# Kernel optimization log

Hardware: AMD Instinct MI355X
Metric: run time of the kernel (lower is better)

Reference implementation:

```python
import jax, jax.numpy as jnp
import numpy as np
from jax import lax

B, T, C, F = 64, 1152, 64, 8
L_DP, N_DP = 24, 12
NUM_CLASSES = 4


def setup_inputs() -> dict:
    key = jax.random.key(0)
    ks = jax.random.split(key, 8)
    num_chunks = T // L_DP
    return {
        "L_norm": jax.random.normal(ks[0], (B, C, C), jnp.float32) / C,
        "X_seq": jax.random.normal(ks[1], (B, T, C, F), jnp.float32),
        "deterministic": 1,
        "conv_kernel": jax.random.normal(ks[2], (32, 1, F, 8), jnp.float32) * 0.06,  # HWIO
        "ln_scale": jnp.ones((8,), jnp.float32),
        "ln_bias": jnp.zeros((8,), jnp.float32),
        "spatial_w": jax.random.normal(ks[3], (64, 4), jnp.float32) * 0.17,
        "W1": jax.random.normal(ks[4], (num_chunks * 64, 32), jnp.float32) * 0.02,
        "b1": jnp.zeros((32,), jnp.float32),
        "W2": jax.random.normal(ks[5], (32, NUM_CLASSES), jnp.float32) * 0.1,
        "b2": jnp.zeros((NUM_CLASSES,), jnp.float32),
    }


def _spike(x):
    return jnp.where(x > 0, 1.0, 0.0).astype(x.dtype)


def reference(L_norm, X_seq, deterministic, conv_kernel, ln_scale, ln_bias,
              spatial_w, W1, b1, W2, b2):
    # temporal conv over (T, C) spatial dims, F -> 8 channels, SAME padding
    ann = lax.conv_general_dilated(
        X_seq, conv_kernel, window_strides=(1, 1), padding="SAME",
        dimension_numbers=("NHWC", "HWIO", "NHWC"))
    # LayerNorm over last (feature) axis, eps=1e-6 (flax default)
    mu = jnp.mean(ann, axis=-1, keepdims=True)
    var = jnp.mean(jnp.square(ann - mu), axis=-1, keepdims=True)
    ann = (ann - mu) * lax.rsqrt(var + 1e-6) * ln_scale + ln_bias
    ann = jax.nn.relu(ann)
    # graph propagation + channel-spatial projection
    gx = jnp.einsum("bnm,btmf->btnf", L_norm, ann)          # (B,T,64,8)
    gx_csp = jnp.einsum("btcf,cs->btsf", gx, spatial_w)     # (B,T,4,8)
    snn_in = gx_csp.reshape(B, T, 32)

    # two-layer LIF recurrence over time (strictly sequential)
    def step(carry, x_t):
        mem1, mem2, mem_out = carry
        mem1 = mem1 * 0.8 + x_t
        spk1 = _spike(mem1 - 0.5)
        mem1 = mem1 - spk1 * 0.5
        mem2 = mem2 * 0.9 + spk1
        spk2 = _spike(mem2 - 0.5)
        mem2 = mem2 - spk2 * 0.5
        mem_out = mem_out * 0.95 + spk2
        return (mem1, mem2, mem_out), (mem_out, spk1, spk2)

    mem0 = jnp.zeros((B, 32), snn_in.dtype)
    _, (pot, spk1, spk2) = lax.scan(step, (mem0, mem0, mem0),
                                    jnp.swapaxes(snn_in, 0, 1))
    pot = jnp.swapaxes(pot, 0, 1)                           # (B,T,32)

    chunks = pot.reshape(B, T // L_DP, L_DP, 32)
    start_mean = jnp.mean(chunks[:, :, :N_DP, :], axis=2)
    end_mean = jnp.mean(chunks[:, :, -N_DP:, :], axis=2)
    flat = jnp.concatenate([start_mean, end_mean], axis=-1).reshape(B, -1)

    y = jax.nn.gelu(flat @ W1 + b1)   # flax nn.gelu default approximate=True
    logits = y @ W2 + b2
    firing_rate = (jnp.mean(spk1) + jnp.mean(spk2)) / 2.0
    return logits, firing_rate
```

## Files before the change

kernel.cpp:

```cpp
#include <hip/hip_runtime.h>
#include <hip/hip_fp16.h>
#include <math.h>

#define T_SEQ 1152

typedef _Float16 f16x8 __attribute__((ext_vector_type(8)));
typedef float f32x4 __attribute__((ext_vector_type(4)));

__global__ void mKernel(const float* __restrict__ L, const float* __restrict__ sw,
                        float* __restrict__ Mbuf) {
  int b = blockIdx.x, tid = threadIdx.x;
  int s = tid >> 6, m = tid & 63;
  float a = 0.f;
  #pragma unroll 4
  for (int n = 0; n < 64; ++n)
    a = fmaf(sw[n * 4 + s], L[(b * 64 + n) * 64 + m], a);
  Mbuf[b * 256 + m * 4 + s] = a;
}

__global__ __launch_bounds__(256, 4)
void convKernel(const float* __restrict__ X, const float* __restrict__ Kw,
                const float* __restrict__ lnS, const float* __restrict__ lnB,
                const float* __restrict__ Mbuf, float* __restrict__ snn) {
  __shared__ int4 XS[4 * 4 * 68];

  const int bid  = blockIdx.x;
  const int b    = bid / 18;
  const int tile = bid - b * 18;
  const int t0   = tile * 64;
  const int tid  = threadIdx.x;
  const int lane = tid & 63;
  const int wid  = tid >> 6;
  const int h    = wid & 1;
  const int g    = wid >> 1;
  const int w32  = h * 32;
  const int tcol = lane & 15;
  const int rg   = lane >> 4;
  const int fA   = lane & 15;

  f16x8 ka[12];
  #pragma unroll
  for (int q = 0; q < 12; ++q) {
    const int kh = 4 * q + rg;
    #pragma unroll
    for (int j = 0; j < 8; ++j) {
      float kv = 0.f;
      if (fA < 8) { if (kh < 32) kv = Kw[kh * 64 + j * 8 + fA]; }
      else { int k2 = kh - 16; if (k2 >= 0 && k2 < 32) kv = Kw[k2 * 64 + j * 8 + fA - 8]; }
      ka[q][j] = (_Float16)kv;
    }
  }

  const float4 lnSlo = *(const float4*)lnS,       lnShi = *(const float4*)(lnS + 4);
  const float4 lnBlo = *(const float4*)lnB,       lnBhi = *(const float4*)(lnB + 4);
  const bool hiQ = (rg & 1);
  const float lnSq[4] = { hiQ ? lnShi.x : lnSlo.x, hiQ ? lnShi.y : lnSlo.y,
                          hiQ ? lnShi.z : lnSlo.z, hiQ ? lnShi.w : lnSlo.w };
  const float lnBq[4] = { hiQ ? lnBhi.x : lnBlo.x, hiQ ? lnBhi.y : lnBlo.y,
                          hiQ ? lnBhi.z : lnBlo.z, hiQ ? lnBhi.w : lnBlo.w };

  const int srow = lane;
  const int stT  = t0 + w32 - 15 + srow;
  const bool sv  = (srow < 63) && (stT >= 0) && (stT < T_SEQ);
  const bool srv = (srow < 63);
  const float* xb = X + (size_t)(b * T_SEQ) * 512;
  int4* wXS = XS + wid * 272;

  #pragma unroll
  for (int c2 = 0; c2 < 4; ++c2) {
    if (srv) {
      float4 a0 = make_float4(0.f,0.f,0.f,0.f), a1 = a0;
      if (sv) {
        const float* p = xb + (size_t)stT * 512 + (g * 4 + c2) * 8;
        a0 = *(const float4*)p; a1 = *(const float4*)(p + 4);
      }
      unsigned u0 = __builtin_bit_cast(unsigned, __float22half2_rn(make_float2(a0.x, a0.y)));
      unsigned u1 = __builtin_bit_cast(unsigned, __float22half2_rn(make_float2(a0.z, a0.w)));
      unsigned u2 = __builtin_bit_cast(unsigned, __float22half2_rn(make_float2(a1.x, a1.y)));
      unsigned u3 = __builtin_bit_cast(unsigned, __float22half2_rn(make_float2(a1.z, a1.w)));
      int4 v; v.x=(int)u0; v.y=(int)u1; v.z=(int)u2; v.w=(int)u3;
      wXS[c2 * 68 + srow] = v;
    }
  }

  float pacc[4][4];
  #pragma unroll
  for (int r = 0; r < 4; ++r)
    #pragma unroll
    for (int s = 0; s < 4; ++s) pacc[r][s] = 0.f;

  #pragma unroll 1
  for (int part = 0; part < 8; ++part) {
    float4 pf0[4], pf1[4];
    if (part < 7) {
      const int chb = (part + 1) * 8 + g * 4;
      #pragma unroll
      for (int c2 = 0; c2 < 4; ++c2) {
        pf0[c2] = make_float4(0.f,0.f,0.f,0.f); pf1[c2] = pf0[c2];
        if (sv) {
          const float* p = xb + (size_t)stT * 512 + (chb + c2) * 8;
          pf0[c2] = *(const float4*)p; pf1[c2] = *(const float4*)(p + 4);
        }
      }
    }

    #pragma unroll 2
    for (int cc = 0; cc < 4; ++cc) {
      f32x4 acc = {0.f, 0.f, 0.f, 0.f};
      const int4* rb = wXS + cc * 68 + tcol + rg;
      #pragma unroll
      for (int q = 0; q < 12; ++q) {
        f16x8 xf = __builtin_bit_cast(f16x8, rb[4 * q]);
        acc = __builtin_amdgcn_mfma_f32_16x16x32_f16(ka[q], xf, acc, 0, 0, 0);
      }
      float s1 = (acc[0] + acc[1]) + (acc[2] + acc[3]);
      float s2 = fmaf(acc[0], acc[0], fmaf(acc[1], acc[1],
                 fmaf(acc[2], acc[2], acc[3] * acc[3])));
      s1 += __shfl_xor(s1, 16, 64);
      s2 += __shfl_xor(s2, 16, 64);
      float mu = s1 * 0.125f;
      float var = fmaf(-mu, mu, s2 * 0.125f);
      float rs = 1.0f / sqrtf(var + 1e-6f);
      const float4 Mc = *(const float4*)(Mbuf + b * 256 + (part * 8 + g * 4 + cc) * 4);
      #pragma unroll
      for (int r = 0; r < 4; ++r) {
        float hr = fmaxf(fmaf((acc[r] - mu) * rs, lnSq[r], lnBq[r]), 0.f);
        pacc[r][0] = fmaf(hr, Mc.x, pacc[r][0]);
        pacc[r][1] = fmaf(hr, Mc.y, pacc[r][1]);
        pacc[r][2] = fmaf(hr, Mc.z, pacc[r][2]);
        pacc[r][3] = fmaf(hr, Mc.w, pacc[r][3]);
      }
    }

    if (part < 7) {
      #pragma unroll
      for (int c2 = 0; c2 < 4; ++c2) {
        if (srv) {
          unsigned u0 = __builtin_bit_cast(unsigned, __float22half2_rn(make_float2(pf0[c2].x, pf0[c2].y)));
          unsigned u1 = __builtin_bit_cast(unsigned, __float22half2_rn(make_float2(pf0[c2].z, pf0[c2].w)));
          unsigned u2 = __builtin_bit_cast(unsigned, __float22half2_rn(make_float2(pf1[c2].x, pf1[c2].y)));
          unsigned u3 = __builtin_bit_cast(unsigned, __float22half2_rn(make_float2(pf1[c2].z, pf1[c2].w)));
          int4 v; v.x=(int)u0; v.y=(int)u1; v.z=(int)u2; v.w=(int)u3;
          wXS[c2 * 68 + srow] = v;
        }
      }
    }
  }

  __syncthreads();
  float* RedF = (float*)&XS[0];
  {
    const int base = (wid * 64 + lane) * 17;
    #pragma unroll
    for (int r = 0; r < 4; ++r)
      #pragma unroll
      for (int s = 0; s < 4; ++s) RedF[base + r * 4 + s] = pacc[r][s];
  }
  __syncthreads();
  {
    const int tt = tid >> 2, s = tid & 3;
    const int hh = tt >> 5, tl15 = tt & 15, rgHi = (tt >> 4) & 1;
    float v[8];
    #pragma unroll
    for (int cc = 0; cc < 8; ++cc) {
      const int flo = cc >> 2, r = cc & 3;
      const int ln = (rgHi * 2 + flo) * 16 + tl15;
      v[cc] = RedF[((0 * 2 + hh) * 64 + ln) * 17 + r * 4 + s]
            + RedF[((1 * 2 + hh) * 64 + ln) * 17 + r * 4 + s];
    }
    float* op = snn + ((size_t)b * T_SEQ + t0 + tt) * 32 + s * 8;
    *(float4*)op       = make_float4(v[0], v[1], v[2], v[3]);
    *(float4*)(op + 4) = make_float4(v[4], v[5], v[6], v[7]);
  }
}

__global__ __launch_bounds__(64, 1)
void scanKernel(const float* __restrict__ snn, float* __restrict__ flat,
                float* __restrict__ spkPart) {
  const int tid = threadIdx.x;
  const int j = tid & 31;
  const int b = blockIdx.x * 2 + (tid >> 5);
  const float* base = snn + (size_t)b * T_SEQ * 32 + j;

  float m1 = 0.f, m2 = 0.f, mo = 0.f, s1 = 0.f, s2 = 0.f;
  float cur[24], nxt[24];
  #pragma unroll
  for (int u = 0; u < 24; ++u) cur[u] = base[(size_t)u * 32];

  #pragma unroll 1
  for (int ch = 0; ch < 48; ++ch) {
    if (ch < 47) {
      #pragma unroll
      for (int u = 0; u < 24; ++u) nxt[u] = base[(size_t)((ch + 1) * 24 + u) * 32];
    }
    float aS = 0.f, aE = 0.f;
    #pragma unroll
    for (int u = 0; u < 24; ++u) {
      m1 = m1 * 0.8f + cur[u];
      float sp1 = (m1 > 0.5f) ? 1.f : 0.f;  m1 -= sp1 * 0.5f;
      m2 = m2 * 0.9f + sp1;
      float sp2 = (m2 > 0.5f) ? 1.f : 0.f;  m2 -= sp2 * 0.5f;
      mo = mo * 0.95f + sp2;
      s1 += sp1; s2 += sp2;
      if (u < 12) aS += mo; else aE += mo;
    }
    flat[b * 3072 + ch * 64 + j]      = aS / 12.0f;
    flat[b * 3072 + ch * 64 + 32 + j] = aE / 12.0f;
    if (ch < 47) {
      #pragma unroll
      for (int u = 0; u < 24; ++u) cur[u] = nxt[u];
    }
  }
  for (int off = 16; off > 0; off >>= 1) {
    s1 += __shfl_down(s1, off, 32);
    s2 += __shfl_down(s2, off, 32);
  }
  if (j == 0) { spkPart[b * 2] = s1; spkPart[b * 2 + 1] = s2; }
}

__global__ void mlpKernel(const float* __restrict__ flat, const float* __restrict__ W1,
                          const float* __restrict__ b1, const float* __restrict__ W2,
                          const float* __restrict__ b2, const float* __restrict__ spkPart,
                          float* __restrict__ out) {
  if (blockIdx.x == 64) {
    if (threadIdx.x == 0) {
      float s1 = 0.f, s2 = 0.f;
      for (int i = 0; i < 64; ++i) { s1 += spkPart[2*i]; s2 += spkPart[2*i+1]; }
      out[256] = (s1 + s2) * 0.5f / (64.0f * 1152.0f * 32.0f);
    }
    return;
  }
  const int b = blockIdx.x;
  const int tid = threadIdx.x;
  const int u = tid & 31, kc = tid >> 5;
  __shared__ float red[256];
  __shared__ float ys[32];
  float p = 0.f;
  const int kbeg = kc * 384, kend = kbeg + 384;
  #pragma unroll 4
  for (int k = kbeg; k < kend; ++k)
    p = fmaf(flat[b*3072 + k], W1[k*32 + u], p);
  red[tid] = p;
  __syncthreads();
  if (kc == 0) {
    float y = b1[u];
    #pragma unroll
    for (int q = 0; q < 8; ++q) y += red[q*32 + u];
    float y3 = y * y * y;
    float th = tanhf(0.7978845608028654f * (y + 0.044715f * y3));
    ys[u] = 0.5f * y * (1.0f + th);
  }
  __syncthreads();
  if (tid < 4) {
    float accv = b2[tid];
    #pragma unroll
    for (int q = 0; q < 32; ++q) accv = fmaf(ys[q], W2[q*4 + tid], accv);
    out[b*4 + tid] = accv;
  }
}

extern "C" void kernel_launch(void* const* d_in, const int* in_sizes, int n_in,
                              void* d_out, int out_size, void* d_ws, size_t ws_size,
                              hipStream_t stream) {
  const float* L   = (const float*)d_in[0];
  const float* X   = (const float*)d_in[1];
  const float* Kw  = (const float*)d_in[3];
  const float* lnS = (const float*)d_in[4];
  const float* lnB = (const float*)d_in[5];
  const float* sw  = (const float*)d_in[6];
  const float* W1  = (const float*)d_in[7];
  const float* b1  = (const float*)d_in[8];
  const float* W2  = (const float*)d_in[9];
  const float* b2  = (const float*)d_in[10];

  float* ws   = (float*)d_ws;
  float* Mbuf = ws;
  float* snn  = Mbuf + 16384;
  float* flat = snn + 2359296;
  float* spk  = flat + 196608;
  float* out  = (float*)d_out;

  mKernel<<<64, 256, 0, stream>>>(L, sw, Mbuf);
  convKernel<<<1152, 256, 0, stream>>>(X, Kw, lnS, lnB, Mbuf, snn);
  scanKernel<<<32, 64, 0, stream>>>(snn, flat, spk);
  mlpKernel<<<65, 256, 0, stream>>>(flat, W1, b1, W2, b2, spk, out);
}
```

Measured before the change: 178.7 us.

## Restructure conv kernel into single-wave blocks with a software-pipelined channel ring

The conv kernel now runs one 64-lane wave per block covering 32 timesteps, looping over all 64 channels itself instead of splitting them across four waves. A ring of eight LDS slots lets the global loads for later channels stay in flight while MFMA work runs on the current one. The kernel-weight layout is remapped so each wave produces whole outputs, which removes the cross-wave LDS reduction and the two block barriers. In exchange the grid doubles, each block reloads overlapping halo rows, and each wave does a longer serial loop with no intra-block parallelism.

```diff
diff --git a/kernel.cpp b/kernel.cpp
--- a/kernel.cpp
+++ b/kernel.cpp
@@ -6,6 +6,11 @@
 
 typedef _Float16 f16x8 __attribute__((ext_vector_type(8)));
 typedef float f32x4 __attribute__((ext_vector_type(4)));
+typedef int   i32x2 __attribute__((ext_vector_type(2)));
+
+__device__ __forceinline__ float pairsum32(float v) {
+  return v + __shfl_xor(v, 32, 64);
+}
 
 __global__ void mKernel(const float* __restrict__ L, const float* __restrict__ sw,
                         float* __restrict__ Mbuf) {
@@ -18,70 +23,51 @@
   Mbuf[b * 256 + m * 4 + s] = a;
 }
 
-__global__ __launch_bounds__(256, 4)
+__global__ __launch_bounds__(64, 4)
 void convKernel(const float* __restrict__ X, const float* __restrict__ Kw,
                 const float* __restrict__ lnS, const float* __restrict__ lnB,
                 const float* __restrict__ Mbuf, float* __restrict__ snn) {
-  __shared__ int4 XS[4 * 4 * 68];
-
-  const int bid  = blockIdx.x;
-  const int b    = bid / 18;
-  const int tile = bid - b * 18;
-  const int t0   = tile * 64;
-  const int tid  = threadIdx.x;
-  const int lane = tid & 63;
-  const int wid  = tid >> 6;
-  const int h    = wid & 1;
-  const int g    = wid >> 1;
-  const int w32  = h * 32;
-  const int tcol = lane & 15;
-  const int rg   = lane >> 4;
-  const int fA   = lane & 15;
-
+  __shared__ int4 XS[8 * 68];
+
+  const int bid   = blockIdx.x;
+  const int b     = bid / 36;
+  const int tile  = bid - b * 36;
+  const int tBase = tile * 32;
+  const int lane  = threadIdx.x;
+  const int tcol  = lane & 15;
+  const int rg    = lane >> 4;
+
+  const int rA = lane & 15;
+  const int fr = ((rA >> 3) << 2) | (rA & 3);
+  const int sh = ((rA >> 2) & 1) << 4;
   f16x8 ka[12];
   #pragma unroll
   for (int q = 0; q < 12; ++q) {
-    const int kh = 4 * q + rg;
+    const int khs = 4 * q + rg - sh;
     #pragma unroll
     for (int j = 0; j < 8; ++j) {
-      float kv = 0.f;
-      if (fA < 8) { if (kh < 32) kv = Kw[kh * 64 + j * 8 + fA]; }
-      else { int k2 = kh - 16; if (k2 >= 0 && k2 < 32) kv = Kw[k2 * 64 + j * 8 + fA - 8]; }
+      float kv = (khs >= 0 && khs < 32) ? Kw[khs * 64 + j * 8 + fr] : 0.f;
       ka[q][j] = (_Float16)kv;
     }
   }
 
-  const float4 lnSlo = *(const float4*)lnS,       lnShi = *(const float4*)(lnS + 4);
-  const float4 lnBlo = *(const float4*)lnB,       lnBhi = *(const float4*)(lnB + 4);
-  const bool hiQ = (rg & 1);
-  const float lnSq[4] = { hiQ ? lnShi.x : lnSlo.x, hiQ ? lnShi.y : lnSlo.y,
-                          hiQ ? lnShi.z : lnSlo.z, hiQ ? lnShi.w : lnSlo.w };
-  const float lnBq[4] = { hiQ ? lnBhi.x : lnBlo.x, hiQ ? lnBhi.y : lnBlo.y,
-                          hiQ ? lnBhi.z : lnBlo.z, hiQ ? lnBhi.w : lnBlo.w };
-
-  const int srow = lane;
-  const int stT  = t0 + w32 - 15 + srow;
-  const bool sv  = (srow < 63) && (stT >= 0) && (stT < T_SEQ);
-  const bool srv = (srow < 63);
-  const float* xb = X + (size_t)(b * T_SEQ) * 512;
-  int4* wXS = XS + wid * 272;
-
-  #pragma unroll
-  for (int c2 = 0; c2 < 4; ++c2) {
-    if (srv) {
-      float4 a0 = make_float4(0.f,0.f,0.f,0.f), a1 = a0;
-      if (sv) {
-        const float* p = xb + (size_t)stT * 512 + (g * 4 + c2) * 8;
-        a0 = *(const float4*)p; a1 = *(const float4*)(p + 4);
-      }
-      unsigned u0 = __builtin_bit_cast(unsigned, __float22half2_rn(make_float2(a0.x, a0.y)));
-      unsigned u1 = __builtin_bit_cast(unsigned, __float22half2_rn(make_float2(a0.z, a0.w)));
-      unsigned u2 = __builtin_bit_cast(unsigned, __float22half2_rn(make_float2(a1.x, a1.y)));
-      unsigned u3 = __builtin_bit_cast(unsigned, __float22half2_rn(make_float2(a1.z, a1.w)));
-      int4 v; v.x=(int)u0; v.y=(int)u1; v.z=(int)u2; v.w=(int)u3;
-      wXS[c2 * 68 + srow] = v;
-    }
-  }
+  const int fb = (rg >> 1) << 2;
+  const float4 lnSq = *(const float4*)(lnS + fb);
+  const float4 lnBq = *(const float4*)(lnB + fb);
+
+  const int half = lane & 1;
+  const int row0 = lane >> 1;
+  const int row1 = row0 + 32;
+  const int tg0 = tBase - 15 + row0;
+  const int tg1 = tBase - 15 + row1;
+  const bool v0 = (tg0 >= 0) && (tg0 < T_SEQ);
+  const bool v1 = (tg1 >= 0) && (tg1 < T_SEQ);
+  const float* xb = X + (size_t)b * T_SEQ * 512 + half * 4;
+  const long a0 = (long)tg0 * 512;
+  const long a1 = (long)tg1 * 512;
+  const size_t lds0 = (size_t)row0 * 16 + half * 8;
+  const size_t lds1 = (size_t)row1 * 16 + half * 8;
+  char* xsb = (char*)&XS[0];
 
   float pacc[4][4];
   #pragma unroll
@@ -89,88 +75,79 @@
     #pragma unroll
     for (int s = 0; s < 4; ++s) pacc[r][s] = 0.f;
 
+  const float4 z4 = make_float4(0.f, 0.f, 0.f, 0.f);
+  float4 pA0, pA1, pB0, pB1;
+
+#define ISSUE(CH, P0, P1)                                                  \
+  { P0 = v0 ? *(const float4*)(xb + a0 + (CH) * 8) : z4;                   \
+    P1 = v1 ? *(const float4*)(xb + a1 + (CH) * 8) : z4; }
+
+#define WRITE(CH, P0, P1)                                                  \
+  { const int slot_ = (CH) & 7;                                            \
+    i32x2 c0, c1;                                                          \
+    c0.x = (int)__builtin_bit_cast(unsigned, __float22half2_rn(make_float2(P0.x, P0.y))); \
+    c0.y = (int)__builtin_bit_cast(unsigned, __float22half2_rn(make_float2(P0.z, P0.w))); \
+    c1.x = (int)__builtin_bit_cast(unsigned, __float22half2_rn(make_float2(P1.x, P1.y))); \
+    c1.y = (int)__builtin_bit_cast(unsigned, __float22half2_rn(make_float2(P1.z, P1.w))); \
+    *(i32x2*)(xsb + slot_ * 1088 + lds0) = c0;                             \
+    *(i32x2*)(xsb + slot_ * 1088 + lds1) = c1; }
+
+#define COMPUTE(CH)                                                        \
+  { const int slot_ = (CH) & 7;                                            \
+    f32x4 acc = {0.f, 0.f, 0.f, 0.f};                                      \
+    const int4* rb = XS + slot_ * 68 + tcol + rg;                          \
+    _Pragma("unroll")                                                      \
+    for (int q = 0; q < 12; ++q) {                                         \
+      f16x8 xf = __builtin_bit_cast(f16x8, rb[4 * q]);                     \
+      acc = __builtin_amdgcn_mfma_f32_16x16x32_f16(ka[q], xf, acc, 0, 0, 0); \
+    }                                                                      \
+    float s1 = (acc[0] + acc[1]) + (acc[2] + acc[3]);                      \
+    float s2 = fmaf(acc[0], acc[0], fmaf(acc[1], acc[1],                   \
+               fmaf(acc[2], acc[2], acc[3] * acc[3])));                    \
+    s1 = pairsum32(s1);                                                    \
+    s2 = pairsum32(s2);                                                    \
+    float mu = s1 * 0.125f;                                                \
+    float var = fmaf(-mu, mu, s2 * 0.125f);                                \
+    float rs = 1.0f / sqrtf(var + 1e-6f);                                  \
+    const float4 Mc = *(const float4*)(Mbuf + b * 256 + (CH) * 4);         \
+    const float lnSa[4] = {lnSq.x, lnSq.y, lnSq.z, lnSq.w};                \
+    const float lnBa[4] = {lnBq.x, lnBq.y, lnBq.z, lnBq.w};                \
+    _Pragma("unroll")                                                      \
+    for (int r = 0; r < 4; ++r) {                                          \
+      float hr = fmaxf(fmaf((acc[r] - mu) * rs, lnSa[r], lnBa[r]), 0.f);   \
+      pacc[r][0] = fmaf(hr, Mc.x, pacc[r][0]);                             \
+      pacc[r][1] = fmaf(hr, Mc.y, pacc[r][1]);                             \
+      pacc[r][2] = fmaf(hr, Mc.z, pacc[r][2]);                             \
+      pacc[r][3] = fmaf(hr, Mc.w, pacc[r][3]);                             \
+    } }
+
+  ISSUE(0, pA0, pA1);
+  ISSUE(1, pB0, pB1);
+  WRITE(0, pA0, pA1);
+  ISSUE(2, pA0, pA1);
+  WRITE(1, pB0, pB1);
+  ISSUE(3, pB0, pB1);
+
   #pragma unroll 1
-  for (int part = 0; part < 8; ++part) {
-    float4 pf0[4], pf1[4];
-    if (part < 7) {
-      const int chb = (part + 1) * 8 + g * 4;
-      #pragma unroll
-      for (int c2 = 0; c2 < 4; ++c2) {
-        pf0[c2] = make_float4(0.f,0.f,0.f,0.f); pf1[c2] = pf0[c2];
-        if (sv) {
-          const float* p = xb + (size_t)stT * 512 + (chb + c2) * 8;
-          pf0[c2] = *(const float4*)p; pf1[c2] = *(const float4*)(p + 4);
-        }
-      }
-    }
-
-    #pragma unroll 2
-    for (int cc = 0; cc < 4; ++cc) {
-      f32x4 acc = {0.f, 0.f, 0.f, 0.f};
-      const int4* rb = wXS + cc * 68 + tcol + rg;
-      #pragma unroll
-      for (int q = 0; q < 12; ++q) {
-        f16x8 xf = __builtin_bit_cast(f16x8, rb[4 * q]);
-        acc = __builtin_amdgcn_mfma_f32_16x16x32_f16(ka[q], xf, acc, 0, 0, 0);
-      }
-      float s1 = (acc[0] + acc[1]) + (acc[2] + acc[3]);
-      float s2 = fmaf(acc[0], acc[0], fmaf(acc[1], acc[1],
-                 fmaf(acc[2], acc[2], acc[3] * acc[3])));
-      s1 += __shfl_xor(s1, 16, 64);
-      s2 += __shfl_xor(s2, 16, 64);
-      float mu = s1 * 0.125f;
-      float var = fmaf(-mu, mu, s2 * 0.125f);
-      float rs = 1.0f / sqrtf(var + 1e-6f);
-      const float4 Mc = *(const float4*)(Mbuf + b * 256 + (part * 8 + g * 4 + cc) * 4);
-      #pragma unroll
-      for (int r = 0; r < 4; ++r) {
-        float hr = fmaxf(fmaf((acc[r] - mu) * rs, lnSq[r], lnBq[r]), 0.f);
-        pacc[r][0] = fmaf(hr, Mc.x, pacc[r][0]);
-        pacc[r][1] = fmaf(hr, Mc.y, pacc[r][1]);
-        pacc[r][2] = fmaf(hr, Mc.z, pacc[r][2]);
-        pacc[r][3] = fmaf(hr, Mc.w, pacc[r][3]);
-      }
-    }
-
-    if (part < 7) {
-      #pragma unroll
-      for (int c2 = 0; c2 < 4; ++c2) {
-        if (srv) {
-          unsigned u0 = __builtin_bit_cast(unsigned, __float22half2_rn(make_float2(pf0[c2].x, pf0[c2].y)));
-          unsigned u1 = __builtin_bit_cast(unsigned, __float22half2_rn(make_float2(pf0[c2].z, pf0[c2].w)));
-          unsigned u2 = __builtin_bit_cast(unsigned, __float22half2_rn(make_float2(pf1[c2].x, pf1[c2].y)));
-          unsigned u3 = __builtin_bit_cast(unsigned, __float22half2_rn(make_float2(pf1[c2].z, pf1[c2].w)));
-          int4 v; v.x=(int)u0; v.y=(int)u1; v.z=(int)u2; v.w=(int)u3;
-          wXS[c2 * 68 + srow] = v;
-        }
-      }
-    }
-  }
-
-  __syncthreads();
-  float* RedF = (float*)&XS[0];
+  for (int s = 0; s < 64; s += 2) {
+    if (s + 2 < 64) WRITE(s + 2, pA0, pA1);
+    if (s + 4 < 64) ISSUE(s + 4, pA0, pA1);
+    COMPUTE(s);
+    if (s + 3 < 64) WRITE(s + 3, pB0, pB1);
+    if (s + 5 < 64) ISSUE(s + 5, pB0, pB1);
+    COMPUTE(s + 1);
+  }
+#undef ISSUE
+#undef WRITE
+#undef COMPUTE
+
   {
-    const int base = (wid * 64 + lane) * 17;
-    #pragma unroll
-    for (int r = 0; r < 4; ++r)
-      #pragma unroll
-      for (int s = 0; s < 4; ++s) RedF[base + r * 4 + s] = pacc[r][s];
-  }
-  __syncthreads();
-  {
-    const int tt = tid >> 2, s = tid & 3;
-    const int hh = tt >> 5, tl15 = tt & 15, rgHi = (tt >> 4) & 1;
-    float v[8];
-    #pragma unroll
-    for (int cc = 0; cc < 8; ++cc) {
-      const int flo = cc >> 2, r = cc & 3;
-      const int ln = (rgHi * 2 + flo) * 16 + tl15;
-      v[cc] = RedF[((0 * 2 + hh) * 64 + ln) * 17 + r * 4 + s]
-            + RedF[((1 * 2 + hh) * 64 + ln) * 17 + r * 4 + s];
-    }
-    float* op = snn + ((size_t)b * T_SEQ + t0 + tt) * 32 + s * 8;
-    *(float4*)op       = make_float4(v[0], v[1], v[2], v[3]);
-    *(float4*)(op + 4) = make_float4(v[4], v[5], v[6], v[7]);
+    const int tloc = tcol + (rg & 1) * 16;
+    float* op = snn + ((size_t)b * T_SEQ + tBase + tloc) * 32;
+    #pragma unroll
+    for (int s = 0; s < 4; ++s)
+      *(float4*)(op + s * 8 + fb) =
+          make_float4(pacc[0][s], pacc[1][s], pacc[2][s], pacc[3][s]);
   }
 }
 
@@ -281,7 +258,7 @@
   float* out  = (float*)d_out;
 
   mKernel<<<64, 256, 0, stream>>>(L, sw, Mbuf);
-  convKernel<<<1152, 256, 0, stream>>>(X, Kw, lnS, lnB, Mbuf, snn);
+  convKernel<<<2304, 64, 0, stream>>>(X, Kw, lnS, lnB, Mbuf, snn);
   scanKernel<<<32, 64, 0, stream>>>(snn, flat, spk);
   mlpKernel<<<65, 256, 0, stream>>>(flat, W1, b1, W2, b2, spk, out);
 }
```

After: 233.0 us. 30.4% more time.

## Share conv input tile across waves and transpose MFMA output through LDS for LayerNorm

Applied to the files above, without the earlier changes.

The conv kernel now loads each 8-channel input slice once per block into a shared LDS tile that all four waves read, instead of every wave loading its own halo copy with register prefetch. The MFMA kernel layout changes so that the accumulator outputs are staged through a second LDS buffer and re-read so each lane holds all 8 features of one (t,c) pair. LayerNorm is then computed in-lane without cross-lane shuffles, and the final reduction uses one shuffle plus a smaller LDS exchange. In exchange, the kernel gains block-wide barriers each part, loses the global-load prefetch overlap, and uses more LDS, which may lower occupancy.

```diff
diff --git a/kernel.cpp b/kernel.cpp
--- a/kernel.cpp
+++ b/kernel.cpp
@@ -22,7 +22,8 @@
 void convKernel(const float* __restrict__ X, const float* __restrict__ Kw,
                 const float* __restrict__ lnS, const float* __restrict__ lnB,
                 const float* __restrict__ Mbuf, float* __restrict__ snn) {
-  __shared__ int4 XS[4 * 4 * 68];
+  __shared__ int4   XS[8 * 97];
+  __shared__ float4 hT4[1024];
 
   const int bid  = blockIdx.x;
   const int b    = bid / 18;
@@ -36,141 +37,137 @@
   const int w32  = h * 32;
   const int tcol = lane & 15;
   const int rg   = lane >> 4;
-  const int fA   = lane & 15;
-
+  const int fq   = rg & 1;
+  const int tloc = tcol + ((rg >> 1) << 4);
+
+  const int rA = lane & 15;
+  const int fr = rA & 7;
+  const int sh16 = (rA >> 3) << 4;
   f16x8 ka[12];
   #pragma unroll
   for (int q = 0; q < 12; ++q) {
-    const int kh = 4 * q + rg;
+    const int khs = 4 * q + rg - sh16;
     #pragma unroll
     for (int j = 0; j < 8; ++j) {
-      float kv = 0.f;
-      if (fA < 8) { if (kh < 32) kv = Kw[kh * 64 + j * 8 + fA]; }
-      else { int k2 = kh - 16; if (k2 >= 0 && k2 < 32) kv = Kw[k2 * 64 + j * 8 + fA - 8]; }
+      float kv = (khs >= 0 && khs < 32) ? Kw[khs * 64 + j * 8 + fr] : 0.f;
       ka[q][j] = (_Float16)kv;
     }
   }
 
-  const float4 lnSlo = *(const float4*)lnS,       lnShi = *(const float4*)(lnS + 4);
-  const float4 lnBlo = *(const float4*)lnB,       lnBhi = *(const float4*)(lnB + 4);
-  const bool hiQ = (rg & 1);
-  const float lnSq[4] = { hiQ ? lnShi.x : lnSlo.x, hiQ ? lnShi.y : lnSlo.y,
-                          hiQ ? lnShi.z : lnSlo.z, hiQ ? lnShi.w : lnSlo.w };
-  const float lnBq[4] = { hiQ ? lnBhi.x : lnBlo.x, hiQ ? lnBhi.y : lnBlo.y,
-                          hiQ ? lnBhi.z : lnBlo.z, hiQ ? lnBhi.w : lnBlo.w };
-
-  const int srow = lane;
-  const int stT  = t0 + w32 - 15 + srow;
-  const bool sv  = (srow < 63) && (stT >= 0) && (stT < T_SEQ);
-  const bool srv = (srow < 63);
+  const int tpt   = lane >> 1;
+  const int cslot = lane & 1;
+
+  const int sc2 = tid & 7;
+  int stl[3]; long gb[3]; bool tv[3];
+  #pragma unroll
+  for (int k = 0; k < 3; ++k) {
+    stl[k] = (tid >> 3) + 32 * k;
+    int tt = t0 - 15 + stl[k];
+    tv[k] = (stl[k] < 95) && (tt >= 0) && (tt < T_SEQ);
+    gb[k] = (long)tt * 512 + sc2 * 8;
+  }
   const float* xb = X + (size_t)(b * T_SEQ) * 512;
-  int4* wXS = XS + wid * 272;
-
-  #pragma unroll
-  for (int c2 = 0; c2 < 4; ++c2) {
-    if (srv) {
-      float4 a0 = make_float4(0.f,0.f,0.f,0.f), a1 = a0;
-      if (sv) {
-        const float* p = xb + (size_t)stT * 512 + (g * 4 + c2) * 8;
-        a0 = *(const float4*)p; a1 = *(const float4*)(p + 4);
-      }
-      unsigned u0 = __builtin_bit_cast(unsigned, __float22half2_rn(make_float2(a0.x, a0.y)));
-      unsigned u1 = __builtin_bit_cast(unsigned, __float22half2_rn(make_float2(a0.z, a0.w)));
-      unsigned u2 = __builtin_bit_cast(unsigned, __float22half2_rn(make_float2(a1.x, a1.y)));
-      unsigned u3 = __builtin_bit_cast(unsigned, __float22half2_rn(make_float2(a1.z, a1.w)));
-      int4 v; v.x=(int)u0; v.y=(int)u1; v.z=(int)u2; v.w=(int)u3;
-      wXS[c2 * 68 + srow] = v;
-    }
-  }
-
-  float pacc[4][4];
-  #pragma unroll
-  for (int r = 0; r < 4; ++r)
-    #pragma unroll
-    for (int s = 0; s < 4; ++s) pacc[r][s] = 0.f;
+
+  float pacc[4][8];
+  #pragma unroll
+  for (int s = 0; s < 4; ++s)
+    #pragma unroll
+    for (int f = 0; f < 8; ++f) pacc[s][f] = 0.f;
 
   #pragma unroll 1
   for (int part = 0; part < 8; ++part) {
-    float4 pf0[4], pf1[4];
-    if (part < 7) {
-      const int chb = (part + 1) * 8 + g * 4;
-      #pragma unroll
-      for (int c2 = 0; c2 < 4; ++c2) {
-        pf0[c2] = make_float4(0.f,0.f,0.f,0.f); pf1[c2] = pf0[c2];
-        if (sv) {
-          const float* p = xb + (size_t)stT * 512 + (chb + c2) * 8;
-          pf0[c2] = *(const float4*)p; pf1[c2] = *(const float4*)(p + 4);
+    #pragma unroll
+    for (int k = 0; k < 3; ++k) {
+      if (stl[k] < 95) {
+        float4 a0 = make_float4(0.f, 0.f, 0.f, 0.f), a1 = a0;
+        if (tv[k]) {
+          const float* p = xb + gb[k] + part * 64;
+          a0 = *(const float4*)p;
+          a1 = *(const float4*)(p + 4);
         }
+        unsigned u0 = __builtin_bit_cast(unsigned, __float22half2_rn(make_float2(a0.x, a0.y)));
+        unsigned u1 = __builtin_bit_cast(unsigned, __float22half2_rn(make_float2(a0.z, a0.w)));
+        unsigned u2 = __builtin_bit_cast(unsigned, __float22half2_rn(make_float2(a1.x, a1.y)));
+        unsigned u3 = __builtin_bit_cast(unsigned, __float22half2_rn(make_float2(a1.z, a1.w)));
+        int4 v; v.x = (int)u0; v.y = (int)u1; v.z = (int)u2; v.w = (int)u3;
+        XS[sc2 * 97 + stl[k]] = v;
       }
     }
+    __syncthreads();
 
     #pragma unroll 2
     for (int cc = 0; cc < 4; ++cc) {
       f32x4 acc = {0.f, 0.f, 0.f, 0.f};
-      const int4* rb = wXS + cc * 68 + tcol + rg;
+      const int rb = (g * 4 + cc) * 97 + w32 + tcol + rg;
       #pragma unroll
       for (int q = 0; q < 12; ++q) {
-        f16x8 xf = __builtin_bit_cast(f16x8, rb[4 * q]);
+        f16x8 xf = __builtin_bit_cast(f16x8, XS[rb + 4 * q]);
         acc = __builtin_amdgcn_mfma_f32_16x16x32_f16(ka[q], xf, acc, 0, 0, 0);
       }
-      float s1 = (acc[0] + acc[1]) + (acc[2] + acc[3]);
-      float s2 = fmaf(acc[0], acc[0], fmaf(acc[1], acc[1],
-                 fmaf(acc[2], acc[2], acc[3] * acc[3])));
-      s1 += __shfl_xor(s1, 16, 64);
-      s2 += __shfl_xor(s2, 16, 64);
-      float mu = s1 * 0.125f;
-      float var = fmaf(-mu, mu, s2 * 0.125f);
-      float rs = 1.0f / sqrtf(var + 1e-6f);
-      const float4 Mc = *(const float4*)(Mbuf + b * 256 + (part * 8 + g * 4 + cc) * 4);
-      #pragma unroll
-      for (int r = 0; r < 4; ++r) {
-        float hr = fmaxf(fmaf((acc[r] - mu) * rs, lnSq[r], lnBq[r]), 0.f);
-        pacc[r][0] = fmaf(hr, Mc.x, pacc[r][0]);
-        pacc[r][1] = fmaf(hr, Mc.y, pacc[r][1]);
-        pacc[r][2] = fmaf(hr, Mc.z, pacc[r][2]);
-        pacc[r][3] = fmaf(hr, Mc.w, pacc[r][3]);
+      float4 st; st.x = acc[0]; st.y = acc[1]; st.z = acc[2]; st.w = acc[3];
+      hT4[wid * 256 + cc * 64 + fq * 32 + tloc] = st;
+    }
+
+    #pragma unroll
+    for (int cc2 = 0; cc2 < 2; ++cc2) {
+      const int c2l = cslot * 2 + cc2;
+      float4 lo = hT4[wid * 256 + c2l * 64 + tpt];
+      float4 hi = hT4[wid * 256 + c2l * 64 + 32 + tpt];
+      float hv[8] = { lo.x, lo.y, lo.z, lo.w, hi.x, hi.y, hi.z, hi.w };
+      float mu = 0.f;
+      #pragma unroll
+      for (int f = 0; f < 8; ++f) mu += hv[f];
+      mu *= 0.125f;
+      float var = 0.f;
+      #pragma unroll
+      for (int f = 0; f < 8; ++f) { float d = hv[f] - mu; hv[f] = d; var = fmaf(d, d, var); }
+      float rs = 1.0f / sqrtf(var * 0.125f + 1e-6f);
+      const int c = part * 8 + g * 4 + c2l;
+      const float4 Mc = *(const float4*)(Mbuf + b * 256 + c * 4);
+      #pragma unroll
+      for (int f = 0; f < 8; ++f) {
+        float hh = fmaxf(fmaf(hv[f] * rs, lnS[f], lnB[f]), 0.f);
+        pacc[0][f] = fmaf(hh, Mc.x, pacc[0][f]);
+        pacc[1][f] = fmaf(hh, Mc.y, pacc[1][f]);
+        pacc[2][f] = fmaf(hh, Mc.z, pacc[2][f]);
+        pacc[3][f] = fmaf(hh, Mc.w, pacc[3][f]);
       }
     }
-
-    if (part < 7) {
-      #pragma unroll
-      for (int c2 = 0; c2 < 4; ++c2) {
-        if (srv) {
-          unsigned u0 = __builtin_bit_cast(unsigned, __float22half2_rn(make_float2(pf0[c2].x, pf0[c2].y)));
-          unsigned u1 = __builtin_bit_cast(unsigned, __float22half2_rn(make_float2(pf0[c2].z, pf0[c2].w)));
-          unsigned u2 = __builtin_bit_cast(unsigned, __float22half2_rn(make_float2(pf1[c2].x, pf1[c2].y)));
-          unsigned u3 = __builtin_bit_cast(unsigned, __float22half2_rn(make_float2(pf1[c2].z, pf1[c2].w)));
-          int4 v; v.x=(int)u0; v.y=(int)u1; v.z=(int)u2; v.w=(int)u3;
-          wXS[c2 * 68 + srow] = v;
-        }
-      }
-    }
-  }
-
+    __syncthreads();
+  }
+
+  #pragma unroll
+  for (int s = 0; s < 4; ++s)
+    #pragma unroll
+    for (int f = 0; f < 8; ++f)
+      pacc[s][f] += __shfl_xor(pacc[s][f], 1, 64);
+
+  float* RedF = (float*)&XS[0];
+  const int trow = h * 32 + tpt;
+  if (g == 0 && cslot == 0) {
+    #pragma unroll
+    for (int s = 0; s < 4; ++s)
+      #pragma unroll
+      for (int f = 0; f < 8; ++f)
+        RedF[trow * 33 + s * 8 + f] = pacc[s][f];
+  }
   __syncthreads();
-  float* RedF = (float*)&XS[0];
-  {
-    const int base = (wid * 64 + lane) * 17;
-    #pragma unroll
-    for (int r = 0; r < 4; ++r)
-      #pragma unroll
-      for (int s = 0; s < 4; ++s) RedF[base + r * 4 + s] = pacc[r][s];
-  }
-  __syncthreads();
-  {
-    const int tt = tid >> 2, s = tid & 3;
-    const int hh = tt >> 5, tl15 = tt & 15, rgHi = (tt >> 4) & 1;
-    float v[8];
-    #pragma unroll
-    for (int cc = 0; cc < 8; ++cc) {
-      const int flo = cc >> 2, r = cc & 3;
-      const int ln = (rgHi * 2 + flo) * 16 + tl15;
-      v[cc] = RedF[((0 * 2 + hh) * 64 + ln) * 17 + r * 4 + s]
-            + RedF[((1 * 2 + hh) * 64 + ln) * 17 + r * 4 + s];
-    }
-    float* op = snn + ((size_t)b * T_SEQ + t0 + tt) * 32 + s * 8;
-    *(float4*)op       = make_float4(v[0], v[1], v[2], v[3]);
-    *(float4*)(op + 4) = make_float4(v[4], v[5], v[6], v[7]);
+  if (g == 1 && cslot == 0) {
+    float* op = snn + ((size_t)b * T_SEQ + t0 + trow) * 32;
+    #pragma unroll
+    for (int s = 0; s < 4; ++s) {
+      float4 v0, v1;
+      v0.x = pacc[s][0] + RedF[trow * 33 + s * 8 + 0];
+      v0.y = pacc[s][1] + RedF[trow * 33 + s * 8 + 1];
+      v0.z = pacc[s][2] + RedF[trow * 33 + s * 8 + 2];
+      v0.w = pacc[s][3] + RedF[trow * 33 + s * 8 + 3];
+      v1.x = pacc[s][4] + RedF[trow * 33 + s * 8 + 4];
+      v1.y = pacc[s][5] + RedF[trow * 33 + s * 8 + 5];
+      v1.z = pacc[s][6] + RedF[trow * 33 + s * 8 + 6];
+      v1.w = pacc[s][7] + RedF[trow * 33 + s * 8 + 7];
+      *(float4*)(op + s * 8)     = v0;
+      *(float4*)(op + s * 8 + 4) = v1;
+    }
   }
 }
 
```

Result: faster. 147.8 us (-17.3%).
